# Performance work log

Hardware: AMD Instinct MI355X
Metric: run time of the kernel (lower is better)

The kernel has to match this reference:

```python
import jax, jax.numpy as jnp
import numpy as np

V, E, SH, H = 30000, 1024, 2048, 1024   # vocab, emb_size, ses_hid_size, hid_size
B, T = 64, 50
PAD = 10003
H2 = 2 * H  # GRU hidden size


def setup_inputs() -> dict:
    key = jax.random.key(0)
    ks = jax.random.split(key, 12)
    s = 0.02
    emb_W = jax.random.normal(ks[2], (V, E), jnp.float32) * s
    emb_W = emb_W.at[PAD].set(0.0)  # padding_idx row is zero
    return {
        "ses_encoding": jax.random.normal(ks[0], (B, 1, SH), jnp.float32),
        "x": jax.random.randint(ks[1], (B, T), 0, V),
        "emb_W": emb_W,
        "gru_Wih": jax.random.normal(ks[3], (3 * H2, E), jnp.float32) * s,
        "gru_Whh": jax.random.normal(ks[4], (3 * H2, H2), jnp.float32) * s,
        "gru_bih": jax.random.normal(ks[5], (3 * H2,), jnp.float32) * s,
        "gru_bhh": jax.random.normal(ks[6], (3 * H2,), jnp.float32) * s,
        "lin1_W": jax.random.normal(ks[7], (H, SH), jnp.float32) * s,
        "lin1_b": jax.random.normal(ks[8], (H,), jnp.float32) * s,
        "lin2_W": jax.random.normal(ks[9], (E, H2), jnp.float32) * s,
        "lin2_b": jax.random.normal(ks[10], (E,), jnp.float32) * s,
        "out_W": jax.random.normal(ks[11], (V, E), jnp.float32) * s,
    }


def reference(ses_encoding, x, emb_W, gru_Wih, gru_Whh, gru_bih, gru_bhh,
              lin1_W, lin1_b, lin2_W, lin2_b, out_W):
    # ses_encoding: [B,1,SH] -> tanh(lin1) -> [B,1,H] -> view [1,B,H] -> [B,H]
    ses = jnp.tanh(jnp.einsum('bos,hs->boh', ses_encoding, lin1_W) + lin1_b)
    ses_enc = ses.reshape(B, H)  # [B, H]

    toks = x.T  # [T, B], teacher-forced inputs
    tok_next = jnp.concatenate([x[:, 1:], jnp.zeros((B, 1), x.dtype)], axis=1).T  # [T, B]
    has_next = jnp.arange(T) < (T - 1)  # [T]

    def step(h, xs):
        tok, nxt, hn = xs  # tok: [B]
        emb = jnp.where((tok == PAD)[:, None], 0.0, emb_W[tok])  # [B, E] (dropout=eval identity)
        hcat = jnp.concatenate([h, ses_enc], axis=-1)  # [B, 2H]
        gi = emb @ gru_Wih.T + gru_bih    # [B, 6H]
        gh = hcat @ gru_Whh.T + gru_bhh   # [B, 6H]
        i_r, i_z, i_n = jnp.split(gi, 3, axis=-1)
        h_r, h_z, h_n = jnp.split(gh, 3, axis=-1)
        r = jax.nn.sigmoid(i_r + h_r)
        z = jax.nn.sigmoid(i_z + h_z)
        n = jnp.tanh(i_n + r * h_n)
        h_full = (1.0 - z) * n + z * hcat     # [B, 2H]
        h_next = h_full[:, :H]                # keep first hid_size half
        hid_o = h_full @ lin2_W.T + lin2_b + emb  # [B, E]
        logits = hid_o @ out_W.T              # [B, V]
        logp = jax.nn.log_softmax(logits, axis=-1)
        ll = jnp.where(hn, logp[jnp.arange(B), nxt], 0.0)  # [B]
        return h_next, (logits, ll)

    _, (all_logits, all_ll) = jax.lax.scan(step, ses_enc, (toks, tok_next, has_next))
    dec_o = jnp.transpose(all_logits, (1, 0, 2))  # [B, T, V]
    log_l = jnp.sum(all_ll, axis=0)               # [B]
    return dec_o, log_l
```

## Files before the change

kernel.cpp:

```cpp
#include <hip/hip_runtime.h>
#include <hip/hip_bf16.h>
#include <stdint.h>

#define VV   30000
#define EE   1024
#define SHH  2048
#define HH   1024
#define H2   2048
#define G3   6144
#define BB   64
#define TT   50
#define PADT 10003
#define MM   3200
#define NPAD 30080
#define RBLK 64
#define PNB  (NPAD / 64)

typedef __bf16 bf16;
typedef bf16  bf16x8 __attribute__((ext_vector_type(8)));
typedef bf16  bf16x4v __attribute__((ext_vector_type(4)));
typedef float f32x4 __attribute__((ext_vector_type(4)));

__device__ __forceinline__ void async16(void* lds_base, const void* gsrc) {
    __builtin_amdgcn_global_load_lds(
        (const __attribute__((address_space(1))) void*)gsrc,
        (__attribute__((address_space(3))) void*)lds_base, 16, 0, 0);
}

__device__ __forceinline__ int xcd_swizzle(int lin, int nwg) {
    int q = nwg >> 3, r = nwg & 7;
    int x = lin & 7, o = lin >> 3;
    return (x < r ? x * (q + 1) : r * (q + 1) + (x - r) * q) + o;
}

__device__ __forceinline__ float sigmoidf_(float x) {
    return 1.f / (1.f + __expf(-x));
}

__global__ __launch_bounds__(256) void k_conv(bf16* dst, const float* src, int n) {
    int i = (blockIdx.x * 256 + threadIdx.x) * 4;
    if (i + 3 >= n) return;
    float4 v = *(const float4*)&src[i];
    bf16x4v o; o[0] = (bf16)v.x; o[1] = (bf16)v.y; o[2] = (bf16)v.z; o[3] = (bf16)v.w;
    *(bf16x4v*)&dst[i] = o;
}

__global__ __launch_bounds__(256) void k_conv_outw(bf16* dst, const float* src) {
    int row = blockIdx.x;
    int c = threadIdx.x * 4;
    bf16x4v o;
    if (row < VV) {
        float4 v = *(const float4*)&src[(size_t)row * EE + c];
        o[0] = (bf16)v.x; o[1] = (bf16)v.y; o[2] = (bf16)v.z; o[3] = (bf16)v.w;
    } else {
        o[0] = (bf16)0.f; o[1] = (bf16)0.f; o[2] = (bf16)0.f; o[3] = (bf16)0.f;
    }
    *(bf16x4v*)&dst[(size_t)row * EE + c] = o;
}

__global__ __launch_bounds__(256) void k_conv_whhhi(bf16* dst, const float* whh) {
    int d = blockIdx.x;
    int cblk = d / 192, rem = d % 192, g = rem / 64, s = rem % 64;
    const float* srow = whh + (size_t)(g * H2 + 1024 + cblk * 64 + s) * H2;
    int c = threadIdx.x * 4;
    float4 v = *(const float4*)&srow[c];
    bf16x4v o; o[0] = (bf16)v.x; o[1] = (bf16)v.y; o[2] = (bf16)v.z; o[3] = (bf16)v.w;
    *(bf16x4v*)&dst[(size_t)d * HH + c] = o;
}

__global__ __launch_bounds__(256) void k_embed(const int* x, const float* embW, bf16* out) {
    int i = blockIdx.x;
    int t = i >> 6, b = i & 63;
    int tok = x[b * TT + t];
    int e = threadIdx.x * 4;
    bf16x4v o;
    if (tok == PADT) {
        o[0] = (bf16)0.f; o[1] = (bf16)0.f; o[2] = (bf16)0.f; o[3] = (bf16)0.f;
    } else {
        float4 v = *(const float4*)&embW[(size_t)tok * EE + e];
        o[0] = (bf16)v.x; o[1] = (bf16)v.y; o[2] = (bf16)v.z; o[3] = (bf16)v.w;
    }
    *(bf16x4v*)&out[(size_t)i * EE + e] = o;
}

template<int KIND>
__global__ __launch_bounds__(256)
void sgemm64(const float* __restrict__ A, const float* __restrict__ Bm,
             const float* __restrict__ bias, float* __restrict__ Of, bf16* __restrict__ Ob,
             int N, int K, int lda, int ldb, int koff, int ldo) {
    int n0 = blockIdx.x * 64;
    int tid = threadIdx.x;
    int tr = tid >> 4, tc = tid & 15;
    __shared__ float As[64][33];
    __shared__ float Bs[64][33];
    float acc[4][4] = {};
    for (int k0 = 0; k0 < K; k0 += 32) {
        #pragma unroll
        for (int q = 0; q < 8; ++q) {
            int p = q * 256 + tid; int r = p >> 5, kk = p & 31;
            As[r][kk] = A[(size_t)r * lda + k0 + kk];
            Bs[r][kk] = Bm[(size_t)(n0 + r) * ldb + koff + k0 + kk];
        }
        __syncthreads();
        #pragma unroll
        for (int kk = 0; kk < 32; ++kk) {
            float a4[4], b4[4];
            #pragma unroll
            for (int i = 0; i < 4; i++) a4[i] = As[tr * 4 + i][kk];
            #pragma unroll
            for (int j = 0; j < 4; j++) b4[j] = Bs[tc * 4 + j][kk];
            #pragma unroll
            for (int i = 0; i < 4; i++)
                #pragma unroll
                for (int j = 0; j < 4; j++) acc[i][j] += a4[i] * b4[j];
        }
        __syncthreads();
    }
    #pragma unroll
    for (int i = 0; i < 4; i++)
        #pragma unroll
        for (int j = 0; j < 4; j++) {
            int row = tr * 4 + i, col = n0 + tc * 4 + j;
            float v = acc[i][j] + bias[col];
            if (KIND == 0) {
                v = tanhf(v);
                Of[(size_t)row * N + col] = v;
                Ob[(size_t)row * ldo + col] = (bf16)v;
            } else {
                Of[(size_t)row * N + col] = v;
            }
        }
}

template<int KIND>
__global__ __launch_bounds__(256)
void gemm128(const bf16* __restrict__ A, const bf16* __restrict__ Bm,
             void* __restrict__ Cout, const float* __restrict__ bias,
             const bf16* __restrict__ addend, float* __restrict__ pm,
             float* __restrict__ ps, int N, int K, int lda, int ldb, int Nreal) {
    int nwg = gridDim.x * gridDim.y;
    int lin = blockIdx.y * gridDim.x + blockIdx.x;
    int wg = xcd_swizzle(lin, nwg);
    int bx = wg % gridDim.x, by = wg / gridDim.x;
    const int n0 = bx * 128;
    const int m0 = by * 128;
    const int tid = threadIdx.x;
    const int w = tid >> 6, l = tid & 63;
    const int wr = w >> 1, wc = w & 1;
    __shared__ bf16 As[128 * 32];
    __shared__ bf16 Bs[128 * 32];
    f32x4 acc[4][4] = {};
    const int lrow = l >> 2;
    const int lk = (l & 3) * 8;
    for (int kt = 0; kt < K; kt += 32) {
        #pragma unroll
        for (int q = 0; q < 2; ++q) {
            int ch = w * 2 + q;
            async16(&As[ch * 512], A + (size_t)(m0 + ch * 16 + lrow) * lda + kt + lk);
            async16(&Bs[ch * 512], Bm + (size_t)(n0 + ch * 16 + lrow) * ldb + kt + lk);
        }
        __syncthreads();
        bf16x8 af[4], bfr[4];
        #pragma unroll
        for (int mi = 0; mi < 4; mi++)
            af[mi] = *(const bf16x8*)&As[(wr * 64 + mi * 16 + (l & 15)) * 32 + (l >> 4) * 8];
        #pragma unroll
        for (int ni = 0; ni < 4; ni++)
            bfr[ni] = *(const bf16x8*)&Bs[(wc * 64 + ni * 16 + (l & 15)) * 32 + (l >> 4) * 8];
        #pragma unroll
        for (int mi = 0; mi < 4; mi++)
            #pragma unroll
            for (int ni = 0; ni < 4; ni++)
                acc[mi][ni] = __builtin_amdgcn_mfma_f32_16x16x32_bf16(af[mi], bfr[ni], acc[mi][ni], 0, 0, 0);
        __syncthreads();
    }
    #pragma unroll
    for (int mi = 0; mi < 4; mi++)
        #pragma unroll
        for (int ni = 0; ni < 4; ni++) {
            int row0 = m0 + wr * 64 + mi * 16 + (l >> 4) * 4;
            int col = n0 + wc * 64 + ni * 16 + (l & 15);
            f32x4 v = acc[mi][ni];
            #pragma unroll
            for (int r = 0; r < 4; r++) {
                int rr = row0 + r;
                float xv = v[r];
                if constexpr (KIND == 0 || KIND == 1) xv += bias[col];
                if constexpr (KIND == 1) xv += (float)addend[(size_t)rr * N + col];
                if constexpr (KIND == 2) {
                    if (col < Nreal) {
                        int t = rr >> 6, b = rr & 63;
                        ((float*)Cout)[((size_t)(b * TT + t)) * VV + col] = xv;
                    }
                } else {
                    ((bf16*)Cout)[(size_t)rr * N + col] = (bf16)xv;
                }
            }
        }
    if constexpr (KIND == 2) {
        #pragma unroll
        for (int mi = 0; mi < 4; mi++) {
            #pragma unroll
            for (int r = 0; r < 4; r++) {
                float m = -1e30f, s = 0.f;
                #pragma unroll
                for (int ni = 0; ni < 4; ni++) {
                    int col = n0 + wc * 64 + ni * 16 + (l & 15);
                    if (col < Nreal) {
                        float v = acc[mi][ni][r];
                        float M = fmaxf(m, v);
                        s = s * __expf(m - M) + __expf(v - M);
                        m = M;
                    }
                }
                #pragma unroll
                for (int off = 1; off < 16; off <<= 1) {
                    float m2 = __shfl_xor(m, off);
                    float s2 = __shfl_xor(s, off);
                    float M = fmaxf(m, m2);
                    s = s * __expf(m - M) + s2 * __expf(m2 - M);
                    m = M;
                }
                if ((l & 15) == 0) {
                    int row = m0 + wr * 64 + mi * 16 + (l >> 4) * 4 + r;
                    size_t pidx = (size_t)row * PNB + (n0 >> 6) + wc;
                    pm[pidx] = m; ps[pidx] = s;
                }
            }
        }
    }
}

__global__ __launch_bounds__(384, 1)
void k_rnn(const float* __restrict__ Whh,
           const bf16* __restrict__ gi_b,
           const float* __restrict__ ghs,
           bf16* __restrict__ hfx,
           uint32_t* __restrict__ ctr) {
    const int blk = blockIdx.x;
    const int c0 = blk * 16;
    const int tid = threadIdx.x;
    const int wv = tid >> 6;
    const int l  = tid & 63;
    const int g  = wv >> 1;
    const int mh = wv & 1;
    const int lc = l & 15, lk = l >> 4;
    __shared__ char h_lds[131072];
    __shared__ float ghl[3][64][17];

    bf16x8 breg[32];
    {
        const float* wrow = Whh + ((size_t)(g * H2 + c0 + lc)) * H2;
        #pragma unroll
        for (int kt = 0; kt < 32; ++kt) {
            const float* p = wrow + kt * 32 + lk * 8;
            float4 v0 = *(const float4*)p;
            float4 v1 = *(const float4*)(p + 4);
            bf16x8 o;
            o[0] = (bf16)v0.x; o[1] = (bf16)v0.y; o[2] = (bf16)v0.z; o[3] = (bf16)v0.w;
            o[4] = (bf16)v1.x; o[5] = (bf16)v1.y; o[6] = (bf16)v1.z; o[7] = (bf16)v1.w;
            breg[kt] = o;
        }
    }
    float pr[4], pz[4], pn[4];
    if (wv < 4) {
        #pragma unroll
        for (int r = 0; r < 4; ++r) {
            int b = wv * 16 + lk * 4 + r;
            size_t base = (size_t)b * G3 + c0 + lc;
            pr[r] = ghs[base];
            pz[r] = ghs[base + H2];
            pn[r] = ghs[base + 2 * H2];
        }
    }

    for (int t = 0; t < TT; ++t) {
        {
            const char* hbase = (const char*)(hfx + (size_t)t * BB * H2);
            #pragma unroll
            for (int i = 0; i < 22; ++i) {
                int wo = i * 6144 + wv * 1024;
                if (wo < 131072) {
                    int o = wo + l * 16;
                    int row = o >> 11, cb = o & 2047;
                    const char* src = hbase + row * 4096 + (cb ^ ((row & 7) << 4));
                    async16(h_lds + wo, src);
                }
            }
        }
        __syncthreads();

        bf16 qr[4], qz[4], qn[4];
        if (wv < 4) {
            const bf16* gp = gi_b + ((size_t)t * BB) * G3;
            #pragma unroll
            for (int r = 0; r < 4; ++r) {
                int b = wv * 16 + lk * 4 + r;
                size_t base = (size_t)b * G3 + c0 + lc;
                qr[r] = gp[base];
                qz[r] = gp[base + H2];
                qn[r] = gp[base + 2 * H2];
            }
        }

        f32x4 acc0 = {}, acc1 = {};
        const int r0 = mh * 32 + lc, r1 = r0 + 16;
        const int sw = (lc & 7) << 4;
        #pragma unroll
        for (int kt = 0; kt < 32; ++kt) {
            int cbyte = kt * 64 + lk * 16;
            bf16x8 a0 = *(const bf16x8*)(h_lds + ((r0 * 2048 + cbyte) ^ sw));
            bf16x8 a1 = *(const bf16x8*)(h_lds + ((r1 * 2048 + cbyte) ^ sw));
            acc0 = __builtin_amdgcn_mfma_f32_16x16x32_bf16(a0, breg[kt], acc0, 0, 0, 0);
            acc1 = __builtin_amdgcn_mfma_f32_16x16x32_bf16(a1, breg[kt], acc1, 0, 0, 0);
        }
        #pragma unroll
        for (int r = 0; r < 4; ++r) {
            ghl[g][mh * 32 + lk * 4 + r][lc]      = acc0[r];
            ghl[g][mh * 32 + 16 + lk * 4 + r][lc] = acc1[r];
        }
        __syncthreads();

        if (wv < 4) {
            #pragma unroll
            for (int r = 0; r < 4; ++r) {
                int b = wv * 16 + lk * 4 + r;
                float hr = ghl[0][b][lc] + pr[r];
                float hz = ghl[1][b][lc] + pz[r];
                float hn = ghl[2][b][lc] + pn[r];
                float rg = sigmoidf_((float)qr[r] + hr);
                float zg = sigmoidf_((float)qz[r] + hz);
                float ng = tanhf((float)qn[r] + rg * hn);
                int hvb = (b * 2048 + (c0 + lc) * 2) ^ ((b & 7) << 4);
                float hv = (float)*(const bf16*)(h_lds + hvb);
                float hf = (1.f - zg) * ng + zg * hv;
                hfx[((size_t)(t + 1) * BB + b) * H2 + c0 + lc] = (bf16)hf;
            }
        }

        if (t != TT - 1) {
            __syncthreads();
            if (tid == 0) {
                __hip_atomic_fetch_add(&ctr[t], 1u, __ATOMIC_RELEASE, __HIP_MEMORY_SCOPE_AGENT);
                while (__hip_atomic_load(&ctr[t], __ATOMIC_RELAXED, __HIP_MEMORY_SCOPE_AGENT) < RBLK)
                    __builtin_amdgcn_s_sleep(2);
                __builtin_amdgcn_fence(__ATOMIC_ACQUIRE, "agent");
            }
            __syncthreads();
        }
    }
}

__global__ __launch_bounds__(256)
void k_hi(const bf16* __restrict__ hfx_,
          const float* __restrict__ ses_f,
          const bf16* __restrict__ Wrh,
          const bf16* __restrict__ gi_b,
          const float* __restrict__ ghs,
          bf16* __restrict__ hfx_out) {
    const int cblk = blockIdx.x;
    const int t    = blockIdx.y;
    const int tid = threadIdx.x;
    const int w = tid >> 6, l = tid & 63;
    __shared__ bf16 As[64 * 32];
    __shared__ bf16 Bs[192 * 32];
    f32x4 acc[12] = {};
    const int lrow = l >> 2;
    const int lk = (l & 3) * 8;
    const bf16* Abase = hfx_ + ((size_t)t * BB) * H2;
    for (int kt = 0; kt < HH; kt += 32) {
        async16(&As[w * 512], Abase + (size_t)(w * 16 + lrow) * H2 + kt + lk);
        #pragma unroll
        for (int q = 0; q < 3; ++q) {
            int cb = w * 3 + q;
            async16(&Bs[cb * 512], Wrh + (size_t)(cblk * 192 + cb * 16 + lrow) * HH + kt + lk);
        }
        __syncthreads();
        bf16x8 af = *(const bf16x8*)&As[(w * 16 + (l & 15)) * 32 + (l >> 4) * 8];
        #pragma unroll
        for (int j = 0; j < 12; j++) {
            bf16x8 bfj = *(const bf16x8*)&Bs[(j * 16 + (l & 15)) * 32 + (l >> 4) * 8];
            acc[j] = __builtin_amdgcn_mfma_f32_16x16x32_bf16(af, bfj, acc[j], 0, 0, 0);
        }
        __syncthreads();
    }
    #pragma unroll
    for (int jc = 0; jc < 4; jc++) {
        int ch = cblk * 64 + jc * 16 + (l & 15);
        #pragma unroll
        for (int r = 0; r < 4; r++) {
            int b = w * 16 + (l >> 4) * 4 + r;
            size_t gb = (size_t)(t * BB + b) * G3 + 1024 + ch;
            size_t sb = (size_t)b * G3 + 1024 + ch;
            float gr = (float)gi_b[gb];
            float gz = (float)gi_b[gb + H2];
            float gn = (float)gi_b[gb + 2 * H2];
            float hr = acc[jc][r]     + ghs[sb];
            float hz = acc[4 + jc][r] + ghs[sb + H2];
            float hn = acc[8 + jc][r] + ghs[sb + 2 * H2];
            float rg = sigmoidf_(gr + hr);
            float zg = sigmoidf_(gz + hz);
            float ng = tanhf(gn + rg * hn);
            float hv = ses_f[b * HH + ch];
            float hf = (1.f - zg) * ng + zg * hv;
            hfx_out[((size_t)(t + 1) * BB + b) * H2 + HH + ch] = (bf16)hf;
        }
    }
}

__global__ void k_lse(const float* __restrict__ pm, const float* __restrict__ ps,
                      const float* __restrict__ logits, const int* __restrict__ x,
                      float* __restrict__ ll) {
    int row = blockIdx.x;
    int t = row >> 6, b = row & 63;
    int l = threadIdx.x;
    float m = -1e30f, s = 0.f;
    for (int i = l; i < PNB; i += 64) {
        float mi = pm[(size_t)row * PNB + i];
        float si = ps[(size_t)row * PNB + i];
        float M = fmaxf(m, mi);
        s = s * __expf(m - M) + si * __expf(mi - M);
        m = M;
    }
    #pragma unroll
    for (int off = 32; off; off >>= 1) {
        float m2 = __shfl_down(m, off);
        float s2 = __shfl_down(s, off);
        float M = fmaxf(m, m2);
        s = s * __expf(m - M) + s2 * __expf(m2 - M);
        m = M;
    }
    if (l == 0) {
        float v = 0.f;
        if (t < TT - 1) {
            int nxt = x[b * TT + t + 1];
            v = logits[((size_t)(b * TT + t)) * VV + nxt] - (m + __logf(s));
        }
        ll[row] = v;
    }
}

__global__ void k_sumll(const float* __restrict__ ll_ws, float* __restrict__ out) {
    int b = threadIdx.x;
    if (b < BB) {
        float s = 0.f;
        for (int t = 0; t < TT; t++) s += ll_ws[t * BB + b];
        out[b] = s;
    }
}

extern "C" void kernel_launch(void* const* d_in, const int* in_sizes, int n_in,
                              void* d_out, int out_size, void* d_ws, size_t ws_size,
                              hipStream_t stream) {
    const float* ses_encoding = (const float*)d_in[0];
    const int*   x            = (const int*)d_in[1];
    const float* emb_W        = (const float*)d_in[2];
    const float* gru_Wih      = (const float*)d_in[3];
    const float* gru_Whh      = (const float*)d_in[4];
    const float* gru_bih      = (const float*)d_in[5];
    const float* gru_bhh      = (const float*)d_in[6];
    const float* lin1_W       = (const float*)d_in[7];
    const float* lin1_b       = (const float*)d_in[8];
    const float* lin2_W       = (const float*)d_in[9];
    const float* lin2_b       = (const float*)d_in[10];
    const float* out_W        = (const float*)d_in[11];

    char* W = (char*)d_ws;
    size_t off = 0;
    auto take = [&](size_t bytes) { void* p = W + off; off += (bytes + 255) & ~(size_t)255; return p; };

    float* ses_f32 = (float*)take((size_t)BB * HH * 4);
    bf16* Wih_b    = (bf16*)take((size_t)G3 * EE * 2);
    bf16* Wrh_b    = (bf16*)take((size_t)3072 * HH * 2);
    bf16* lin2_b16 = (bf16*)take((size_t)EE * H2 * 2);
    bf16* outW_b   = (bf16*)take((size_t)NPAD * EE * 2);
    bf16* emb_b    = (bf16*)take((size_t)MM * EE * 2);
    bf16* gi_b     = (bf16*)take((size_t)MM * G3 * 2);
    float* ghs     = (float*)take((size_t)BB * G3 * 4);
    bf16* hfx      = (bf16*)take((size_t)(TT + 1) * BB * H2 * 2);
    bf16* hido_b   = (bf16*)take((size_t)MM * EE * 2);
    float* ll_ws   = (float*)take((size_t)MM * 4);
    float* pm      = (float*)take((size_t)MM * PNB * 4);
    float* ps      = (float*)take((size_t)MM * PNB * 4);
    uint32_t* ctr  = (uint32_t*)take((size_t)TT * 4);

    hipMemsetAsync(ctr, 0, TT * 4, stream);

    k_conv<<<(G3 * EE) / 1024, 256, 0, stream>>>(Wih_b, gru_Wih, G3 * EE);
    k_conv<<<(EE * H2) / 1024, 256, 0, stream>>>(lin2_b16, lin2_W, EE * H2);
    k_conv_outw<<<NPAD, 256, 0, stream>>>(outW_b, out_W);
    k_conv_whhhi<<<3072, 256, 0, stream>>>(Wrh_b, gru_Whh);
    k_embed<<<MM, 256, 0, stream>>>(x, emb_W, emb_b);

    sgemm64<0><<<HH / 64, 256, 0, stream>>>(ses_encoding, lin1_W, lin1_b, ses_f32, hfx,
                                            HH, SHH, SHH, SHH, 0, H2);
    sgemm64<1><<<G3 / 64, 256, 0, stream>>>(ses_f32, gru_Whh, gru_bhh, ghs, nullptr,
                                            G3, HH, HH, H2, HH, 0);

    gemm128<0><<<dim3(G3 / 128, MM / 128), 256, 0, stream>>>(
        emb_b, Wih_b, gi_b, gru_bih, nullptr, nullptr, nullptr, G3, EE, EE, EE, 0);

    k_rnn<<<RBLK, 384, 0, stream>>>(gru_Whh, gi_b, ghs, hfx, ctr);

    k_hi<<<dim3(16, TT), 256, 0, stream>>>(hfx, ses_f32, Wrh_b, gi_b, ghs, hfx);

    gemm128<1><<<dim3(EE / 128, MM / 128), 256, 0, stream>>>(
        hfx + (size_t)BB * H2, lin2_b16, hido_b, lin2_b, emb_b, nullptr, nullptr,
        EE, H2, H2, H2, 0);

    gemm128<2><<<dim3(NPAD / 128, MM / 128), 256, 0, stream>>>(
        hido_b, outW_b, d_out, nullptr, nullptr, pm, ps, NPAD, EE, EE, EE, VV);

    k_lse<<<MM, 64, 0, stream>>>(pm, ps, (const float*)d_out, x, ll_ws);
    k_sumll<<<1, 64, 0, stream>>>(ll_ws, (float*)d_out + (size_t)BB * TT * VV);
}
```

Baseline: 1.565 ms.

## Replace release/acquire fences with relaxed agent-scope atomics in persistent GRU loop

```diff
diff --git a/kernel.cpp b/kernel.cpp
--- a/kernel.cpp
+++ b/kernel.cpp
@@ -275,21 +275,6 @@
     }
 
     for (int t = 0; t < TT; ++t) {
-        {
-            const char* hbase = (const char*)(hfx + (size_t)t * BB * H2);
-            #pragma unroll
-            for (int i = 0; i < 22; ++i) {
-                int wo = i * 6144 + wv * 1024;
-                if (wo < 131072) {
-                    int o = wo + l * 16;
-                    int row = o >> 11, cb = o & 2047;
-                    const char* src = hbase + row * 4096 + (cb ^ ((row & 7) << 4));
-                    async16(h_lds + wo, src);
-                }
-            }
-        }
-        __syncthreads();
-
         bf16 qr[4], qz[4], qn[4];
         if (wv < 4) {
             const bf16* gp = gi_b + ((size_t)t * BB) * G3;
@@ -302,6 +287,31 @@
                 qn[r] = gp[base + 2 * H2];
             }
         }
+
+        {
+            const uint64_t* hsrc = (const uint64_t*)(hfx + (size_t)t * BB * H2);
+            #pragma unroll 1
+            for (int i0 = 0; i0 < 48; i0 += 16) {
+                uint64_t v[16];
+                #pragma unroll
+                for (int j = 0; j < 16; ++j) {
+                    int idx = (i0 + j) * 384 + tid;
+                    v[j] = (idx < 16384)
+                        ? __hip_atomic_load(hsrc + idx, __ATOMIC_RELAXED, __HIP_MEMORY_SCOPE_AGENT)
+                        : 0ull;
+                }
+                #pragma unroll
+                for (int j = 0; j < 16; ++j) {
+                    int idx = (i0 + j) * 384 + tid;
+                    if (idx < 16384) {
+                        int byte = idx * 8;
+                        int swb = byte ^ (((byte >> 11) & 7) << 4);
+                        *(uint64_t*)(h_lds + swb) = v[j];
+                    }
+                }
+            }
+        }
+        __syncthreads();
 
         f32x4 acc0 = {}, acc1 = {};
         const int r0 = mh * 32 + lc, r1 = r0 + 16;
@@ -334,17 +344,20 @@
                 int hvb = (b * 2048 + (c0 + lc) * 2) ^ ((b & 7) << 4);
                 float hv = (float)*(const bf16*)(h_lds + hvb);
                 float hf = (1.f - zg) * ng + zg * hv;
-                hfx[((size_t)(t + 1) * BB + b) * H2 + c0 + lc] = (bf16)hf;
+                union { bf16 h; uint16_t u; } cv;
+                cv.h = (bf16)hf;
+                __hip_atomic_store(
+                    (uint16_t*)&hfx[((size_t)(t + 1) * BB + b) * H2 + c0 + lc],
+                    cv.u, __ATOMIC_RELAXED, __HIP_MEMORY_SCOPE_AGENT);
             }
         }
 
         if (t != TT - 1) {
             __syncthreads();
             if (tid == 0) {
-                __hip_atomic_fetch_add(&ctr[t], 1u, __ATOMIC_RELEASE, __HIP_MEMORY_SCOPE_AGENT);
+                __hip_atomic_fetch_add(&ctr[t], 1u, __ATOMIC_RELAXED, __HIP_MEMORY_SCOPE_AGENT);
                 while (__hip_atomic_load(&ctr[t], __ATOMIC_RELAXED, __HIP_MEMORY_SCOPE_AGENT) < RBLK)
-                    __builtin_amdgcn_s_sleep(2);
-                __builtin_amdgcn_fence(__ATOMIC_ACQUIRE, "agent");
+                    __builtin_amdgcn_s_sleep(1);
             }
             __syncthreads();
         }
```

Result: no change. 1.540 ms (-1.6%).
